# Kernel optimization log

Measured on AMD Instinct MI355X. Metric: run time of the kernel, lower is better.

The kernel has to match this reference:

```python
import jax, jax.numpy as jnp
import numpy as np

EMBED_DIM = 768


def setup_inputs() -> dict:
    key = jax.random.key(0)
    k1, k2, k3, k4, k5 = jax.random.split(key, 5)
    C = EMBED_DIM
    B, N = 32, 1024
    s = 1.0 / np.sqrt(C)
    x = jax.random.normal(k1, (B, N, C), dtype=jnp.float32)
    qkv_w = jax.random.normal(k2, (C, 3 * C), dtype=jnp.float32) * s  # [in, out]
    qkv_b = jax.random.normal(k3, (3 * C,), dtype=jnp.float32) * 0.02
    proj_w = jax.random.normal(k4, (C, C), dtype=jnp.float32) * s
    proj_b = jax.random.normal(k5, (C,), dtype=jnp.float32) * 0.02
    return {"x": x, "qkv_w": qkv_w, "qkv_b": qkv_b, "proj_w": proj_w, "proj_b": proj_b}


def reference(x, qkv_w, qkv_b, proj_w, proj_b):
    B, N, C = x.shape
    qkv = (x @ qkv_w + qkv_b).reshape(B, N, 3, C)
    q, k, v = qkv[:, :, 0], qkv[:, :, 1], qkv[:, :, 2]  # each [B, N, C]
    # single-head full attention; scale by sqrt(C) as in source
    scores = jnp.einsum('bnc,bmc->bnm', q, k) / jnp.sqrt(jnp.asarray(C, x.dtype))
    attn = jax.nn.softmax(scores, axis=-1)  # dropout p=0.0 -> identity
    out = jnp.einsum('bnm,bmc->bnc', attn, v)
    # faithful to source: transpose(1,2).reshape(B,N,C) permutes the data
    out = jnp.swapaxes(out, 1, 2).reshape(B, N, C)
    return out @ proj_w + proj_b
```

## Files before the change

### kernel.cpp

```cpp
#include <hip/hip_runtime.h>
#include <hip/hip_bf16.h>


#define BM 256
#define BN 256
#define BKK 32

typedef __attribute__((ext_vector_type(8))) short bf16x8;
typedef __attribute__((ext_vector_type(4))) float f32x4;

__device__ __forceinline__ unsigned short f2b(float f) {
  unsigned int u = __float_as_uint(f);
  u = u + 0x7fffu + ((u >> 16) & 1u);
  return (unsigned short)(u >> 16);
}

__device__ __forceinline__ void g2l16(const void* g, void* l) {
  __builtin_amdgcn_global_load_lds(
      (const __attribute__((address_space(1))) unsigned int*)g,
      (__attribute__((address_space(3))) unsigned int*)l, 16, 0, 0);
}

template <int EPI>
__global__ __launch_bounds__(512, 2) void gemm_nt8(
    const unsigned short* __restrict__ A, const unsigned short* __restrict__ B,
    unsigned short* __restrict__ Cb, unsigned short* __restrict__ Ck,
    unsigned short* __restrict__ Cv, float* __restrict__ Cf,
    const float* __restrict__ bias, float* __restrict__ Z, int K, int lda,
    int ldb, int ldc, long bsA, long bsB, long bsC, float scale, int MT,
    int NN) {
  __shared__ unsigned short As[2][BM][BKK];
  __shared__ unsigned short Bs[2][BN][BKK];

  const int id = blockIdx.x;
  const int w = (id & 7) * ((int)gridDim.x >> 3) + (id >> 3);
  const int pb = MT * NN;
  const int bz = w / pb;
  const int r = w - bz * pb;
  const int bym = r / NN;
  const int bxn = r - bym * NN;

  const unsigned short* Ag = A + (long)bz * bsA + (long)(bym * BM) * lda;
  const unsigned short* Bg = B + (long)bz * bsB + (long)(bxn * BN) * ldb;

  const int tid = threadIdx.x;
  const int wave = tid >> 6;
  const int lane = tid & 63;
  const int l15 = lane & 15;
  const int lk = lane >> 4;
  const int wm = (wave >> 2) << 7;
  const int wn = (wave & 3) << 6;

  const int sr = lane >> 2;
  const int sc = lane & 3;

  f32x4 acc[8][4];
#pragma unroll
  for (int m = 0; m < 8; ++m)
#pragma unroll
    for (int n = 0; n < 4; ++n)
#pragma unroll
      for (int p = 0; p < 4; ++p) acc[m][n][p] = 0.f;

  auto stA = [&](int d, int k0) {
#pragma unroll
    for (int i = 0; i < 2; ++i) {
      const int rb = (wave << 5) + (i << 4);
      g2l16(Ag + (long)(rb + sr) * lda + k0 + (sc << 3), &As[d][rb][0]);
    }
  };
  auto stB = [&](int d, int k0) {
#pragma unroll
    for (int i = 0; i < 2; ++i) {
      const int rb = (wave << 5) + (i << 4);
      g2l16(Bg + (long)(rb + sr) * ldb + k0 + (sc << 3), &Bs[d][rb][0]);
    }
  };
  auto ldA = [&](int d, int m) {
    return *(const bf16x8*)&As[d][wm + (m << 4) + l15][lk << 3];
  };
  auto ldB = [&](int d, int n) {
    return *(const bf16x8*)&Bs[d][wn + (n << 4) + l15][lk << 3];
  };

  const int NT = K / BKK;
  stA(0, 0); stB(0, 0);
  stA(1, BKK); stB(1, BKK);
  asm volatile("s_waitcnt vmcnt(4)" ::: "memory");
  __builtin_amdgcn_sched_barrier(0);
  __builtin_amdgcn_s_barrier();
  __builtin_amdgcn_sched_barrier(0);

  int cur = 0;
  for (int t = 0; t < NT; ++t) {
    const bool st2 = (t + 2 < NT);
    const int k2 = (t + 2) * BKK;

    bf16x8 bf[4], af[8];
#pragma unroll
    for (int n = 0; n < 4; ++n) bf[n] = ldB(cur, n);
#pragma unroll
    for (int m = 0; m < 8; ++m) af[m] = ldA(cur, m);

    __builtin_amdgcn_s_setprio(1);
#pragma unroll
    for (int m = 0; m < 8; ++m)
#pragma unroll
      for (int n = 0; n < 4; ++n)
        acc[m][n] = __builtin_amdgcn_mfma_f32_16x16x32_bf16(
            af[m], bf[n], acc[m][n], 0, 0, 0);
    __builtin_amdgcn_s_setprio(0);

    __builtin_amdgcn_s_barrier();
    __builtin_amdgcn_sched_barrier(0);
    if (st2) { stB(cur, k2); stA(cur, k2); }
    if (st2)
      asm volatile("s_waitcnt vmcnt(4)" ::: "memory");
    else
      asm volatile("s_waitcnt vmcnt(0)" ::: "memory");
    __builtin_amdgcn_sched_barrier(0);
    __builtin_amdgcn_s_barrier();
    __builtin_amdgcn_sched_barrier(0);
    cur ^= 1;
  }

  const int row0 = bym * BM + wm + (lk << 2);
  const int col0 = bxn * BN + wn;

  if constexpr (EPI == 1) {
    const int seg = (bxn * BN) / 768;
    unsigned short* O = (seg == 0) ? Cb : ((seg == 1) ? Ck : Cv);
    float bv2[4];
#pragma unroll
    for (int n = 0; n < 4; ++n) bv2[n] = bias[col0 + (n << 4) + l15];
    const int cl0 = col0 + l15 - seg * 768;
#pragma unroll
    for (int m = 0; m < 8; ++m)
#pragma unroll
      for (int p = 0; p < 4; ++p) {
        const long rr = row0 + (m << 4) + p;
#pragma unroll
        for (int n = 0; n < 4; ++n)
          O[rr * 768 + cl0 + (n << 4)] = f2b(acc[m][n][p] + bv2[n]);
      }
  } else if constexpr (EPI == 2) {
    float bv2[4];
#pragma unroll
    for (int n = 0; n < 4; ++n) bv2[n] = bias[col0 + (n << 4) + l15];
#pragma unroll
    for (int m = 0; m < 8; ++m)
#pragma unroll
      for (int p = 0; p < 4; ++p) {
        const long rr = row0 + (m << 4) + p;
#pragma unroll
        for (int n = 0; n < 4; ++n)
          Cf[rr * ldc + col0 + (n << 4) + l15] = acc[m][n][p] + bv2[n];
      }
  } else if constexpr (EPI == 3) {
    unsigned short* C = Cb + (long)bz * bsC;
#pragma unroll
    for (int m = 0; m < 8; ++m) {
      float es[4] = {0.f, 0.f, 0.f, 0.f};
#pragma unroll
      for (int p = 0; p < 4; ++p) {
        const long rr = row0 + (m << 4) + p;
#pragma unroll
        for (int n = 0; n < 4; ++n) {
          const float e = __expf(acc[m][n][p] * scale);
          es[p] += e;
          C[rr * ldc + col0 + (n << 4) + l15] = f2b(e);
        }
      }
#pragma unroll
      for (int p = 0; p < 4; ++p) {
        float s = es[p];
        s += __shfl_xor(s, 1);
        s += __shfl_xor(s, 2);
        s += __shfl_xor(s, 4);
        s += __shfl_xor(s, 8);
        if (l15 == 0)
          atomicAdd(&Z[(long)bz * 1024 + row0 + (m << 4) + p], s);
      }
    }
  } else {
    unsigned short* C = Cb + (long)bz * bsC;
    float zv[4];
#pragma unroll
    for (int n = 0; n < 4; ++n)
      zv[n] = 1.f / Z[(long)bz * 1024 + col0 + (n << 4) + l15];
#pragma unroll
    for (int m = 0; m < 8; ++m)
#pragma unroll
      for (int p = 0; p < 4; ++p) {
        const long rr = row0 + (m << 4) + p;
#pragma unroll
        for (int n = 0; n < 4; ++n)
          C[rr * ldc + col0 + (n << 4) + l15] = f2b(acc[m][n][p] * zv[n]);
      }
  }
}

__global__ __launch_bounds__(256) void prep(
    const float4* __restrict__ x, ushort4* __restrict__ x_bf,
    const float* __restrict__ qkv_w, unsigned short* __restrict__ Wqkv,
    const float* __restrict__ proj_w, unsigned short* __restrict__ Wp) {
  const int blk = blockIdx.x;
  if (blk < 24576) {
    const long i = (long)blk * 256 + threadIdx.x;
    float4 f = x[i];
    ushort4 o;
    o.x = f2b(f.x); o.y = f2b(f.y); o.z = f2b(f.z); o.w = f2b(f.w);
    x_bf[i] = o;
  } else if (blk < 24576 + 6912) {
    const long i = (long)(blk - 24576) * 256 + threadIdx.x;
    const int k = (int)(i % 768);
    const int j = (int)(i / 768);
    Wqkv[i] = f2b(qkv_w[(long)k * 2304 + j]);
  } else {
    const long i = (long)(blk - 24576 - 6912) * 256 + threadIdx.x;
    const int k = (int)(i % 768);
    const int j = (int)(i / 768);
    Wp[i] = f2b(proj_w[(long)k * 768 + j]);
  }
}

__global__ __launch_bounds__(256) void transpose_v(
    const unsigned short* __restrict__ V, unsigned short* __restrict__ Vt) {
  __shared__ unsigned short T[64][72];
  const int b = blockIdx.z;
  const int d0 = blockIdx.x << 6;
  const int m0 = blockIdx.y << 6;
  const unsigned short* Vb = V + (long)b * 786432;
  unsigned short* Vtb = Vt + (long)b * 786432;
  const int tid = threadIdx.x;
  const int r = tid >> 2;
  const int c4 = tid & 3;
#pragma unroll
  for (int h = 0; h < 2; ++h) {
    const int cc = (c4 + (h << 2)) << 3;
    *(uint4*)&T[r][cc] = *(const uint4*)&Vb[(long)(m0 + r) * 768 + d0 + cc];
  }
  __syncthreads();
#pragma unroll
  for (int h = 0; h < 2; ++h) {
    const int mm = (c4 + (h << 2)) << 3;
    alignas(16) unsigned short tmp[8];
#pragma unroll
    for (int e = 0; e < 8; ++e) tmp[e] = T[mm + e][r];
    *(uint4*)&Vtb[(long)(d0 + r) * 1024 + m0 + mm] = *(uint4*)tmp;
  }
}

extern "C" void kernel_launch(void* const* d_in, const int* in_sizes, int n_in,
                              void* d_out, int out_size, void* d_ws,
                              size_t ws_size, hipStream_t stream) {
  const float* x = (const float*)d_in[0];
  const float* qkv_w = (const float*)d_in[1];
  const float* qkv_b = (const float*)d_in[2];
  const float* proj_w = (const float*)d_in[3];
  const float* proj_b = (const float*)d_in[4];
  float* out = (float*)d_out;

  char* ws = (char*)d_ws;
  unsigned short* x_bf = (unsigned short*)ws;
  unsigned short* Wqkv = (unsigned short*)(ws + 50331648);
  unsigned short* Wp = (unsigned short*)(ws + 53870592);
  unsigned short* Qb = (unsigned short*)(ws + 55050240);
  unsigned short* Kb = (unsigned short*)(ws + 105381888);
  unsigned short* Vb = (unsigned short*)(ws + 155713536);
  unsigned short* Sb = (unsigned short*)(ws + 206045184);
  unsigned short* Vt = x_bf;
  unsigned short* Hb = Qb;
  float* Zs = (float*)Vb;

  prep<<<33792, 256, 0, stream>>>((const float4*)x, (ushort4*)x_bf, qkv_w,
                                  Wqkv, proj_w, Wp);

  gemm_nt8<1><<<1152, 512, 0, stream>>>(
      x_bf, Wqkv, Qb, Kb, Vb, nullptr, qkv_b, nullptr, 768, 768, 768, 0, 0, 0,
      0, 1.f, 128, 9);

  transpose_v<<<dim3(12, 16, 32), 256, 0, stream>>>(Vb, Vt);

  hipMemsetAsync(Zs, 0, 32 * 1024 * sizeof(float), stream);

  gemm_nt8<3><<<512, 512, 0, stream>>>(
      Qb, Kb, Sb, nullptr, nullptr, nullptr, nullptr, Zs, 768, 768, 768, 1024,
      786432, 786432, 1048576, 0.03608439182435161f, 4, 4);

  gemm_nt8<4><<<384, 512, 0, stream>>>(
      Vt, Sb, Hb, nullptr, nullptr, nullptr, nullptr, Zs, 1024, 1024, 1024,
      1024, 786432, 1048576, 786432, 1.f, 3, 4);

  gemm_nt8<2><<<384, 512, 0, stream>>>(
      Hb, Wp, nullptr, nullptr, nullptr, out, proj_b, nullptr, 768, 768, 768,
      768, 0, 0, 0, 1.f, 128, 3);
}
```

Baseline: 629.9 us.

## Restructure GEMM main loop into eight-phase pipeline with swizzled LDS and BK 64

Result: faster. 568.0 us (-9.8%).

```diff
diff --git a/kernel.cpp b/kernel.cpp
--- a/kernel.cpp
+++ b/kernel.cpp
@@ -4,7 +4,7 @@
 
 #define BM 256
 #define BN 256
-#define BKK 32
+#define BKK 64
 
 typedef __attribute__((ext_vector_type(8))) short bf16x8;
 typedef __attribute__((ext_vector_type(4))) float f32x4;
@@ -29,8 +29,8 @@
     const float* __restrict__ bias, float* __restrict__ Z, int K, int lda,
     int ldb, int ldc, long bsA, long bsB, long bsC, float scale, int MT,
     int NN) {
-  __shared__ unsigned short As[2][BM][BKK];
-  __shared__ unsigned short Bs[2][BN][BKK];
+  __shared__ unsigned short As[2][2][BM][32];
+  __shared__ unsigned short Bs[2][2][BN][32];
 
   const int id = blockIdx.x;
   const int w = (id & 7) * ((int)gridDim.x >> 3) + (id >> 3);
@@ -52,7 +52,7 @@
   const int wn = (wave & 3) << 6;
 
   const int sr = lane >> 2;
-  const int sc = lane & 3;
+  const int scq = (lane & 3) ^ (sr & 3);
 
   f32x4 acc[8][4];
 #pragma unroll
@@ -62,67 +62,92 @@
 #pragma unroll
       for (int p = 0; p < 4; ++p) acc[m][n][p] = 0.f;
 
-  auto stA = [&](int d, int k0) {
+  auto stA = [&](int b, int s, int k0) {
 #pragma unroll
     for (int i = 0; i < 2; ++i) {
       const int rb = (wave << 5) + (i << 4);
-      g2l16(Ag + (long)(rb + sr) * lda + k0 + (sc << 3), &As[d][rb][0]);
+      g2l16(Ag + (long)(rb + sr) * lda + k0 + (s << 5) + (scq << 3),
+            &As[b][s][rb][0]);
     }
   };
-  auto stB = [&](int d, int k0) {
+  auto stB = [&](int b, int s, int k0) {
 #pragma unroll
     for (int i = 0; i < 2; ++i) {
       const int rb = (wave << 5) + (i << 4);
-      g2l16(Bg + (long)(rb + sr) * ldb + k0 + (sc << 3), &Bs[d][rb][0]);
+      g2l16(Bg + (long)(rb + sr) * ldb + k0 + (s << 5) + (scq << 3),
+            &Bs[b][s][rb][0]);
     }
   };
-  auto ldA = [&](int d, int m) {
-    return *(const bf16x8*)&As[d][wm + (m << 4) + l15][lk << 3];
+  auto ldA = [&](int b, int s, int m) {
+    return *(const bf16x8*)&As[b][s][wm + (m << 4) + l15]
+                              [((lk ^ (l15 & 3)) << 3)];
   };
-  auto ldB = [&](int d, int n) {
-    return *(const bf16x8*)&Bs[d][wn + (n << 4) + l15][lk << 3];
+  auto ldB = [&](int b, int s, int n) {
+    return *(const bf16x8*)&Bs[b][s][wn + (n << 4) + l15]
+                              [((lk ^ (l15 & 3)) << 3)];
   };
 
   const int NT = K / BKK;
-  stA(0, 0); stB(0, 0);
-  stA(1, BKK); stB(1, BKK);
-  asm volatile("s_waitcnt vmcnt(4)" ::: "memory");
+  const int NIT = NT >> 1;
+
+  stA(0, 0, 0); stA(0, 1, 0); stB(0, 0, 0); stB(0, 1, 0);
+  stB(1, 0, BKK); stA(1, 0, BKK); stB(1, 1, BKK);
+  asm volatile("s_waitcnt vmcnt(6)" ::: "memory");
   __builtin_amdgcn_sched_barrier(0);
   __builtin_amdgcn_s_barrier();
   __builtin_amdgcn_sched_barrier(0);
 
-  int cur = 0;
-  for (int t = 0; t < NT; ++t) {
-    const bool st2 = (t + 2 < NT);
-    const int k2 = (t + 2) * BKK;
-
-    bf16x8 bf[4], af[8];
-#pragma unroll
-    for (int n = 0; n < 4; ++n) bf[n] = ldB(cur, n);
-#pragma unroll
-    for (int m = 0; m < 8; ++m) af[m] = ldA(cur, m);
-
-    __builtin_amdgcn_s_setprio(1);
-#pragma unroll
-    for (int m = 0; m < 8; ++m)
-#pragma unroll
-      for (int n = 0; n < 4; ++n)
-        acc[m][n] = __builtin_amdgcn_mfma_f32_16x16x32_bf16(
-            af[m], bf[n], acc[m][n], 0, 0, 0);
-    __builtin_amdgcn_s_setprio(0);
-
-    __builtin_amdgcn_s_barrier();
-    __builtin_amdgcn_sched_barrier(0);
-    if (st2) { stB(cur, k2); stA(cur, k2); }
-    if (st2)
-      asm volatile("s_waitcnt vmcnt(4)" ::: "memory");
-    else
-      asm volatile("s_waitcnt vmcnt(0)" ::: "memory");
-    __builtin_amdgcn_sched_barrier(0);
-    __builtin_amdgcn_s_barrier();
-    __builtin_amdgcn_sched_barrier(0);
-    cur ^= 1;
-  }
+  bf16x8 bf[4], af[4];
+
+#define PHASE(b, s, mh, RDB, STAGE_STMT, VM_STMT)                          \
+  {                                                                        \
+    if (RDB) {                                                             \
+      _Pragma("unroll") for (int n = 0; n < 4; ++n) bf[n] = ldB(b, s, n);  \
+    }                                                                      \
+    _Pragma("unroll") for (int m = 0; m < 4; ++m) af[m] =                  \
+        ldA(b, s, (mh << 2) + m);                                          \
+    STAGE_STMT;                                                            \
+    __builtin_amdgcn_sched_barrier(0);                                     \
+    __builtin_amdgcn_s_barrier();                                          \
+    asm volatile("s_waitcnt lgkmcnt(0)" ::: "memory");                     \
+    __builtin_amdgcn_sched_barrier(0);                                     \
+    __builtin_amdgcn_s_setprio(1);                                         \
+    _Pragma("unroll") for (int m = 0; m < 4; ++m)                          \
+      _Pragma("unroll") for (int n = 0; n < 4; ++n)                        \
+        acc[(mh << 2) + m][n] = __builtin_amdgcn_mfma_f32_16x16x32_bf16(   \
+            af[m], bf[n], acc[(mh << 2) + m][n], 0, 0, 0);                 \
+    __builtin_amdgcn_s_setprio(0);                                         \
+    VM_STMT;                                                               \
+    __builtin_amdgcn_s_barrier();                                          \
+  }
+
+  for (int k = 0; k < NIT; ++k) {
+    const bool g = (k + 1 < NIT);
+    const int kt1 = (2 * k + 1) * BKK;
+    const int ku0 = (2 * k + 2) * BKK;
+    const int ku1 = (2 * k + 3) * BKK;
+
+    PHASE(0, 0, 0, true, { stA(1, 1, kt1); }, {});
+    PHASE(0, 0, 1, false, { if (g) stB(0, 0, ku0); }, {});
+    PHASE(0, 1, 0, true, { if (g) stA(0, 0, ku0); }, {});
+    PHASE(0, 1, 1, false, { if (g) stB(0, 1, ku0); }, {
+      if (g)
+        asm volatile("s_waitcnt vmcnt(6)" ::: "memory");
+      else
+        asm volatile("s_waitcnt vmcnt(0)" ::: "memory");
+      __builtin_amdgcn_sched_barrier(0);
+    });
+    PHASE(1, 0, 0, true, { if (g) stA(0, 1, ku0); }, {});
+    PHASE(1, 0, 1, false, { if (g) stB(1, 0, ku1); }, {});
+    PHASE(1, 1, 0, true, { if (g) stA(1, 0, ku1); }, {});
+    PHASE(1, 1, 1, false, { if (g) stB(1, 1, ku1); }, {
+      if (g) {
+        asm volatile("s_waitcnt vmcnt(6)" ::: "memory");
+        __builtin_amdgcn_sched_barrier(0);
+      }
+    });
+  }
+#undef PHASE
 
   const int row0 = bym * BM + wm + (lk << 2);
   const int col0 = bxn * BN + wn;
```
